# Kernel optimization log

Measured on AMD Instinct MI355X. Metric: run time of the kernel, lower is better.

## Reference

```python
import jax, jax.numpy as jnp
import numpy as np

EPS = 1e-06


def _conv1x1(x, W, b):
    # x: [B,C,H,W], W: [O,C], b: [O] -> [B,O,H,W]
    return jnp.einsum('oc,bchw->bohw', W, x) + b[None, :, None, None]


def _l2_norm(x):
    # normalize over channel dim (-2) per position, matching torch.norm(p=2, dim=-2)
    return x / jnp.linalg.norm(x, axis=-2, keepdims=True)


def setup_inputs() -> dict:
    key = jax.random.key(0)
    ks = jax.random.split(key, 8)
    B, C, H, W = 8, 512, 64, 64
    Cq = C // 8
    s = 0.02
    return {
        'x': jax.random.normal(ks[0], (B, C, H, W), jnp.float32),
        'Wq': jax.random.normal(ks[1], (Cq, C), jnp.float32) * s,
        'bq': jax.random.normal(ks[2], (Cq,), jnp.float32) * s,
        'Wk': jax.random.normal(ks[3], (Cq, C), jnp.float32) * s,
        'bk': jax.random.normal(ks[4], (Cq,), jnp.float32) * s,
        'Wv': jax.random.normal(ks[5], (C, C), jnp.float32) * s,
        'bv': jax.random.normal(ks[6], (C,), jnp.float32) * s,
        'gamma': jax.random.normal(ks[7], (1,), jnp.float32),
    }


def reference(x, Wq, bq, Wk, bk, Wv, bv, gamma):
    B, C, H, W = x.shape
    N = H * W
    Q = _conv1x1(x, Wq, bq).reshape(B, -1, N)   # [B,C',N]
    K = _conv1x1(x, Wk, bk).reshape(B, -1, N)   # [B,C',N]
    V = _conv1x1(x, Wv, bv).reshape(B, C, N)    # [B,C,N]

    Qn = _l2_norm(Q).transpose(0, 2, 1)         # [B,N,C']
    Kn = _l2_norm(K)                            # [B,C',N]

    # taylor denominator: 1 / (N + Q . (sum_n K + eps))
    tailor_sum = 1.0 / (N + jnp.einsum('bnc,bc->bn', Qn, Kn.sum(-1) + EPS))  # [B,N]

    value_sum = V.sum(-1)                        # [B,C]
    matrix = jnp.einsum('bmn,bcn->bmc', Kn, V)   # [B,C',C]
    matrix_sum = value_sum[:, :, None] + jnp.einsum('bnm,bmc->bcn', Qn, matrix)  # [B,C,N]

    weight_value = (matrix_sum * tailor_sum[:, None, :]).reshape(B, C, H, W)
    return gamma * weight_value
```

## Files before the change

kernel.cpp:

```cpp
#include <hip/hip_runtime.h>
#include <math.h>

#define B_   8
#define C_   512
#define CQ   64
#define N_   4096
#define EPSF 1e-6f
#define LS   40
#define LS2  72

typedef short  shortx8 __attribute__((ext_vector_type(8)));
typedef short  shortx4 __attribute__((ext_vector_type(4)));
typedef short  shortx2 __attribute__((ext_vector_type(2)));
typedef float  floatx4 __attribute__((ext_vector_type(4)));

__device__ __forceinline__ short f2bf(float f) {
    unsigned u = __builtin_bit_cast(unsigned, f);
    u += 0x7FFFu + ((u >> 16) & 1u);
    return (short)(u >> 16);
}
__device__ __forceinline__ float bf2f(short h) {
    unsigned u = ((unsigned)(unsigned short)h) << 16;
    return __builtin_bit_cast(float, u);
}
__device__ __forceinline__ shortx8 ldf8(const short* p) {
    return *(const shortx8*)p;
}

__global__ __launch_bounds__(256) void pcast(
    const float* __restrict__ Wq, const float* __restrict__ Wk,
    const float* __restrict__ Wv, short* __restrict__ Wqk, short* __restrict__ Wvb)
{
    int i = (blockIdx.x * 256 + threadIdx.x) * 4;
    float4 v; short* dst;
    if (i < 2 * CQ * C_) {
        const float* src = (i < CQ * C_) ? (Wq + i) : (Wk + i - CQ * C_);
        v = *(const float4*)src;
        dst = Wqk + i;
    } else {
        int j = i - 2 * CQ * C_;
        v = *(const float4*)(Wv + j);
        dst = Wvb + j;
    }
    const float* f = (const float*)&v;
    shortx4 o = { f2bf(f[0]), f2bf(f[1]), f2bf(f[2]), f2bf(f[3]) };
    *(shortx4*)dst = o;
}

__global__ __launch_bounds__(256, 2) void k1_qk(
    const float* __restrict__ x, const short* __restrict__ Wqk,
    const float* __restrict__ bq, const float* __restrict__ bk,
    short* __restrict__ Qnt, short* __restrict__ Kn, float* __restrict__ Ksum)
{
    const int b   = blockIdx.y;
    const int n0  = blockIdx.x * 64;
    const int tid = threadIdx.x;
    const int lane = tid & 63, wid = tid >> 6;
    const int waveM = wid >> 1, waveN = wid & 1;
    const int quad = lane >> 4, ln = lane & 15;

    __shared__ short A_l[2][128][LS];
    __shared__ short B_l[2][64][LS];
    __shared__ float bias_l[128];

    if (tid < 128) bias_l[tid] = (tid < 64) ? bq[tid] : bk[tid - 64];

    const int mA = tid >> 1, koA = (tid & 1) * 16;
    const short* Asrc = Wqk + (size_t)mA * C_;
    const int kp = tid >> 4, nq = tid & 15;
    const float* xb = x + (size_t)b * C_ * N_;

    shortx8 a0 = *(const shortx8*)(Asrc + koA);
    shortx8 a1 = *(const shortx8*)(Asrc + koA + 8);
    float4 r0, r1;
    {
        const float* Bs = xb + (size_t)(kp * 2) * N_ + n0 + nq * 4;
        r0 = *(const float4*)(Bs);
        r1 = *(const float4*)(Bs + N_);
    }

    auto stage = [&](int buf, shortx8 s0, shortx8 s1, float4 q0, float4 q1) {
        *(shortx8*)&A_l[buf][mA][koA]     = s0;
        *(shortx8*)&A_l[buf][mA][koA + 8] = s1;
        const float* f0 = (const float*)&q0;
        const float* f1 = (const float*)&q1;
#pragma unroll
        for (int i = 0; i < 4; i++) {
            shortx2 t = { f2bf(f0[i]), f2bf(f1[i]) };
            *(shortx2*)&B_l[buf][nq * 4 + i][kp * 2] = t;
        }
    };
    stage(0, a0, a1, r0, r1);
    __syncthreads();

    const floatx4 z4 = {0.f, 0.f, 0.f, 0.f};
    floatx4 acc[4][2];
#pragma unroll
    for (int mt = 0; mt < 4; mt++) { acc[mt][0] = z4; acc[mt][1] = z4; }

    int cur = 0;
    for (int it = 0; it < 16; ++it) {
        shortx8 na0, na1; float4 nr0, nr1;
        if (it < 15) {
            const int k0 = (it + 1) * 32;
            na0 = *(const shortx8*)(Asrc + k0 + koA);
            na1 = *(const shortx8*)(Asrc + k0 + koA + 8);
            const float* Bs = xb + (size_t)(k0 + kp * 2) * N_ + n0 + nq * 4;
            nr0 = *(const float4*)(Bs);
            nr1 = *(const float4*)(Bs + N_);
        }
        shortx8 af[4];
#pragma unroll
        for (int mt = 0; mt < 4; mt++)
            af[mt] = ldf8(&A_l[cur][waveM * 64 + mt * 16 + ln][quad * 8]);
#pragma unroll
        for (int nt = 0; nt < 2; nt++) {
            shortx8 bf8 = ldf8(&B_l[cur][waveN * 32 + nt * 16 + ln][quad * 8]);
#pragma unroll
            for (int mt = 0; mt < 4; mt++)
                acc[mt][nt] = __builtin_amdgcn_mfma_f32_16x16x32_bf16(af[mt], bf8, acc[mt][nt], 0, 0, 0);
        }
        if (it < 15) stage(cur ^ 1, na0, na1, nr0, nr1);
        __syncthreads();
        cur ^= 1;
    }

#pragma unroll
    for (int mt = 0; mt < 4; mt++)
#pragma unroll
        for (int r = 0; r < 4; r++) {
            float bias = bias_l[waveM * 64 + mt * 16 + quad * 4 + r];
#pragma unroll
            for (int nt = 0; nt < 2; nt++) acc[mt][nt][r] += bias;
        }
#pragma unroll
    for (int nt = 0; nt < 2; nt++) {
        float s = 0.f;
#pragma unroll
        for (int mt = 0; mt < 4; mt++)
#pragma unroll
            for (int r = 0; r < 4; r++) s += acc[mt][nt][r] * acc[mt][nt][r];
        s += __shfl_xor(s, 16);
        s += __shfl_xor(s, 32);
        float inv = rsqrtf(s);
#pragma unroll
        for (int mt = 0; mt < 4; mt++)
#pragma unroll
            for (int r = 0; r < 4; r++) acc[mt][nt][r] *= inv;
    }

    if (waveM == 0) {
        short* Qb = Qnt + (size_t)b * N_ * CQ;
#pragma unroll
        for (int nt = 0; nt < 2; nt++) {
            int n = n0 + waveN * 32 + nt * 16 + ln;
#pragma unroll
            for (int mt = 0; mt < 4; mt++) {
                shortx4 v;
#pragma unroll
                for (int r = 0; r < 4; r++) v[r] = f2bf(acc[mt][nt][r]);
                *(shortx4*)(Qb + (size_t)n * CQ + mt * 16 + quad * 4) = v;
            }
        }
    } else {
        short* Kb = Kn + (size_t)b * CQ * N_;
#pragma unroll
        for (int mt = 0; mt < 4; mt++)
#pragma unroll
            for (int r = 0; r < 4; r++) {
                int m = mt * 16 + quad * 4 + r;
                float s = 0.f;
#pragma unroll
                for (int nt = 0; nt < 2; nt++) {
                    int n = n0 + waveN * 32 + nt * 16 + ln;
                    float v = acc[mt][nt][r];
                    Kb[(size_t)m * N_ + n] = f2bf(v);
                    s += v;
                }
                s += __shfl_xor(s, 1); s += __shfl_xor(s, 2);
                s += __shfl_xor(s, 4); s += __shfl_xor(s, 8);
                if (ln == 0) atomicAdd(&Ksum[b * CQ + m], s);
            }
    }
}

__global__ __launch_bounds__(256, 2) void k2_kx(
    const float* __restrict__ x, const short* __restrict__ Kn,
    float* __restrict__ KX, float* __restrict__ xsum)
{
    const int jt = blockIdx.x, ks = blockIdx.y, b = blockIdx.z;
    const int j0 = jt * 64, nbase = ks * 512;
    const int tid = threadIdx.x;
    const int lane = tid & 63, wid = tid >> 6;
    const int quad = lane >> 4, ln = lane & 15;

    __shared__ short A_l[2][64][LS];
    __shared__ short B_l[2][64][LS];

    const int rA = tid >> 2, oA = (tid & 3) * 8;
    const short* Kb = Kn + (size_t)b * CQ * N_;
    const float* xb = x + (size_t)b * C_ * N_;
    const short* As = Kb + (size_t)rA * N_ + nbase + oA;
    const float* Bs = xb + (size_t)(j0 + rA) * N_ + nbase + oA;

    float xsacc = 0.f;

    shortx8 aC = *(const shortx8*)As;
    float4 b0 = *(const float4*)(Bs);
    float4 b1 = *(const float4*)(Bs + 4);

    auto stage = [&](int buf, shortx8 a, float4 q0, float4 q1) {
        *(shortx8*)&A_l[buf][rA][oA] = a;
        const float* f0 = (const float*)&q0;
        const float* f1 = (const float*)&q1;
        shortx8 t;
#pragma unroll
        for (int i = 0; i < 4; i++) {
            t[i]     = f2bf(f0[i]); xsacc += f0[i];
            t[i + 4] = f2bf(f1[i]); xsacc += f1[i];
        }
        *(shortx8*)&B_l[buf][rA][oA] = t;
    };
    stage(0, aC, b0, b1);
    __syncthreads();

    const floatx4 z4 = {0.f, 0.f, 0.f, 0.f};
    floatx4 acc[4] = {z4, z4, z4, z4};

    int cur = 0;
    for (int it = 0; it < 16; ++it) {
        shortx8 aN; float4 n0v, n1v;
        if (it < 15) {
            const int off = (it + 1) * 32;
            aN  = *(const shortx8*)(As + off);
            n0v = *(const float4*)(Bs + off);
            n1v = *(const float4*)(Bs + off + 4);
        }
        shortx8 af[4];
#pragma unroll
        for (int mt = 0; mt < 4; mt++)
            af[mt] = ldf8(&A_l[cur][mt * 16 + ln][quad * 8]);
        shortx8 bf8 = ldf8(&B_l[cur][wid * 16 + ln][quad * 8]);
#pragma unroll
        for (int mt = 0; mt < 4; mt++)
            acc[mt] = __builtin_amdgcn_mfma_f32_16x16x32_bf16(af[mt], bf8, acc[mt], 0, 0, 0);
        if (it < 15) stage(cur ^ 1, aN, n0v, n1v);
        __syncthreads();
        cur ^= 1;
    }

    xsacc += __shfl_xor(xsacc, 1);
    xsacc += __shfl_xor(xsacc, 2);
    if ((tid & 3) == 0) atomicAdd(&xsum[b * C_ + j0 + rA], xsacc);

    float* KXb = KX + (size_t)b * CQ * C_;
#pragma unroll
    for (int mt = 0; mt < 4; mt++)
#pragma unroll
        for (int r = 0; r < 4; r++) {
            int m = mt * 16 + quad * 4 + r;
            atomicAdd(&KXb[(size_t)m * C_ + j0 + wid * 16 + ln], acc[mt][r]);
        }
}

__global__ __launch_bounds__(256, 2) void k3_m(
    const float* __restrict__ KX, const short* __restrict__ Wvb,
    const float* __restrict__ bv, const float* __restrict__ Ksum,
    const float* __restrict__ xsum,
    short* __restrict__ Mt, float* __restrict__ vs)
{
    const int ct = blockIdx.x, b = blockIdx.y;
    const int c0 = ct * 64;
    const int tid = threadIdx.x;
    const int lane = tid & 63, wid = tid >> 6;
    const int quad = lane >> 4, ln = lane & 15;

    __shared__ short A_l[2][64][LS];
    __shared__ short B_l[2][64][LS];
    __shared__ float xsl[C_], Ksl[64], bvl[64], vsp[4][64];

    xsl[tid] = xsum[(size_t)b * C_ + tid];
    xsl[tid + 256] = xsum[(size_t)b * C_ + tid + 256];
    if (tid < 64) { Ksl[tid] = Ksum[b * CQ + tid]; bvl[tid] = bv[c0 + tid]; }

    const int rA = tid >> 2, oA = (tid & 3) * 8;
    const short* As = Wvb + (size_t)(c0 + rA) * C_ + oA;
    const float* Bs = KX + ((size_t)b * CQ + rA) * C_ + oA;

    shortx8 aC = *(const shortx8*)As;
    float4 b0 = *(const float4*)(Bs);
    float4 b1 = *(const float4*)(Bs + 4);

    auto stage = [&](int buf, shortx8 a, float4 q0, float4 q1) {
        *(shortx8*)&A_l[buf][rA][oA] = a;
        const float* f0 = (const float*)&q0;
        const float* f1 = (const float*)&q1;
        shortx8 t;
#pragma unroll
        for (int i = 0; i < 4; i++) { t[i] = f2bf(f0[i]); t[i + 4] = f2bf(f1[i]); }
        *(shortx8*)&B_l[buf][rA][oA] = t;
    };
    stage(0, aC, b0, b1);
    __syncthreads();

    const floatx4 z4 = {0.f, 0.f, 0.f, 0.f};
    floatx4 acc[4] = {z4, z4, z4, z4};
    float vsacc = 0.f;
    const int cv = tid & 63;

    int cur = 0;
    for (int it = 0; it < 16; ++it) {
        shortx8 aN; float4 n0v, n1v;
        if (it < 15) {
            const int off = (it + 1) * 32;
            aN  = *(const shortx8*)(As + off);
            n0v = *(const float4*)(Bs + off);
            n1v = *(const float4*)(Bs + off + 4);
        }
        shortx8 af[4];
#pragma unroll
        for (int ct2 = 0; ct2 < 4; ct2++)
            af[ct2] = ldf8(&A_l[cur][ct2 * 16 + ln][quad * 8]);
        shortx8 bf8 = ldf8(&B_l[cur][wid * 16 + ln][quad * 8]);
#pragma unroll
        for (int ct2 = 0; ct2 < 4; ct2++)
            acc[ct2] = __builtin_amdgcn_mfma_f32_16x16x32_bf16(af[ct2], bf8, acc[ct2], 0, 0, 0);
#pragma unroll
        for (int jj = 0; jj < 8; jj++)
            vsacc += bf2f(A_l[cur][cv][wid * 8 + jj]) * xsl[it * 32 + wid * 8 + jj];
        if (it < 15) stage(cur ^ 1, aN, n0v, n1v);
        __syncthreads();
        cur ^= 1;
    }

    vsp[wid][cv] = vsacc;
    __syncthreads();
    if (tid < 64)
        vs[(size_t)b * C_ + c0 + tid] =
            vsp[0][tid] + vsp[1][tid] + vsp[2][tid] + vsp[3][tid] + (float)N_ * bvl[tid];

    const int m = wid * 16 + ln;
    const float ksm = Ksl[m];
    short* Mb = Mt + (size_t)b * C_ * CQ;
#pragma unroll
    for (int ct2 = 0; ct2 < 4; ct2++)
#pragma unroll
        for (int r = 0; r < 4; r++) {
            int c = ct2 * 16 + quad * 4 + r;
            Mb[(size_t)(c0 + c) * CQ + m] = f2bf(acc[ct2][r] + ksm * bvl[c]);
        }
}

__global__ __launch_bounds__(256, 2) void k4_out(
    const short* __restrict__ Qnt, const short* __restrict__ Mt,
    const float* __restrict__ vs, const float* __restrict__ Ksum,
    const float* __restrict__ gamma, float* __restrict__ out)
{
    const int nt = blockIdx.x, ct = blockIdx.y, b = blockIdx.z;
    const int n0 = nt * 128, c0 = ct * 128;
    const int tid = threadIdx.x;
    const int lane = tid & 63, wid = tid >> 6;
    const int waveC = wid >> 1, waveN = wid & 1;
    const int quad = lane >> 4, ln = lane & 15;

    __shared__ short A_l[128][LS2];
    __shared__ short B_l[128][LS2];
    __shared__ float tsl[128], vsl[128], Ks_l[64];

    {
        int c = tid >> 1, h = tid & 1;
        const short* src = Mt + ((size_t)b * C_ + c0 + c) * CQ + h * 32;
#pragma unroll
        for (int q = 0; q < 4; q++)
            *(shortx8*)&A_l[c][h * 32 + q * 8] = *(const shortx8*)(src + q * 8);
    }
    {
        int n = tid >> 1, h = tid & 1;
        const short* src = Qnt + ((size_t)b * N_ + n0 + n) * CQ + h * 32;
#pragma unroll
        for (int q = 0; q < 4; q++)
            *(shortx8*)&B_l[n][h * 32 + q * 8] = *(const shortx8*)(src + q * 8);
    }
    if (tid < 64)  Ks_l[tid] = Ksum[b * CQ + tid];
    if (tid < 128) vsl[tid]  = vs[(size_t)b * C_ + c0 + tid];
    __syncthreads();

    if (tid < 128) {
        const short* row = B_l[tid];
        float s = 0.f;
#pragma unroll
        for (int m = 0; m < 64; m++) s += bf2f(row[m]) * (Ks_l[m] + EPSF);
        tsl[tid] = 1.f / ((float)N_ + s);
    }
    __syncthreads();

    const floatx4 z4 = {0.f, 0.f, 0.f, 0.f};
    floatx4 acc[4][4];
#pragma unroll
    for (int i = 0; i < 4; i++)
#pragma unroll
        for (int j = 0; j < 4; j++) acc[i][j] = z4;

#pragma unroll
    for (int kc = 0; kc < 2; kc++) {
        shortx8 af[4];
#pragma unroll
        for (int ct2 = 0; ct2 < 4; ct2++)
            af[ct2] = ldf8(&A_l[waveC * 64 + ct2 * 16 + ln][kc * 32 + quad * 8]);
#pragma unroll
        for (int nt2 = 0; nt2 < 4; nt2++) {
            shortx8 bf8 = ldf8(&B_l[waveN * 64 + nt2 * 16 + ln][kc * 32 + quad * 8]);
#pragma unroll
            for (int ct2 = 0; ct2 < 4; ct2++)
                acc[ct2][nt2] = __builtin_amdgcn_mfma_f32_16x16x32_bf16(af[ct2], bf8, acc[ct2][nt2], 0, 0, 0);
        }
    }

    const float g = gamma[0];
    float* ob = out + (size_t)b * C_ * N_;
#pragma unroll
    for (int ct2 = 0; ct2 < 4; ct2++)
#pragma unroll
        for (int r = 0; r < 4; r++) {
            int cl = waveC * 64 + ct2 * 16 + quad * 4 + r;
            float vc = vsl[cl];
#pragma unroll
            for (int nt2 = 0; nt2 < 4; nt2++) {
                int nl = waveN * 64 + nt2 * 16 + ln;
                ob[(size_t)(c0 + cl) * N_ + n0 + nl] = g * tsl[nl] * (vc + acc[ct2][nt2][r]);
            }
        }
}

extern "C" void kernel_launch(void* const* d_in, const int* in_sizes, int n_in,
                              void* d_out, int out_size, void* d_ws, size_t ws_size,
                              hipStream_t stream)
{
    (void)in_sizes; (void)n_in; (void)out_size; (void)ws_size;
    const float* x     = (const float*)d_in[0];
    const float* Wq    = (const float*)d_in[1];
    const float* bq    = (const float*)d_in[2];
    const float* Wk    = (const float*)d_in[3];
    const float* bk    = (const float*)d_in[4];
    const float* Wv    = (const float*)d_in[5];
    const float* bv    = (const float*)d_in[6];
    const float* gamma = (const float*)d_in[7];
    float* out = (float*)d_out;

    short* Qnt = (short*)d_ws;
    short* Kn  = Qnt + (size_t)B_ * N_ * CQ;
    float* Ksum = (float*)(Kn + (size_t)B_ * CQ * N_);
    float* xsum = Ksum + B_ * CQ;
    float* KX   = xsum + B_ * C_;
    short* Mt   = (short*)(KX + (size_t)B_ * CQ * C_);
    float* vs   = (float*)(Mt + (size_t)B_ * C_ * CQ);
    short* Wqk  = (short*)(vs + B_ * C_);
    short* Wvb  = Wqk + 2 * CQ * C_;

    size_t zbytes = (size_t)(B_ * CQ + B_ * C_ + B_ * CQ * C_) * 4;
    hipMemsetAsync(Ksum, 0, zbytes, stream);

    pcast <<<dim3(320),      256, 0, stream>>>(Wq, Wk, Wv, Wqk, Wvb);
    k1_qk <<<dim3(64, 8),    256, 0, stream>>>(x, Wqk, bq, bk, Qnt, Kn, Ksum);
    k2_kx <<<dim3(8, 8, 8),  256, 0, stream>>>(x, Kn, KX, xsum);
    k3_m  <<<dim3(8, 8),     256, 0, stream>>>(KX, Wvb, bv, Ksum, xsum, Mt, vs);
    k4_out<<<dim3(32, 4, 8), 256, 0, stream>>>(Qnt, Mt, vs, Ksum, gamma, out);
}
```

Measured before the change: 184.0 us.

## Stage full x tile in LDS upfront and read weights directly from global in k1/k2

k1_qk and k2_kx no longer run a double-buffered K loop with a sync every step. They first load and convert the whole x slab (all 512 K values) into a large padded LDS buffer, sync once, then run the MFMA loop, fetching the A operand (Wqk or Kn) straight from global or cache into registers. This removes 16 barriers per block and the A-operand LDS staging. In exchange it uses about 70KB of LDS per block, which may cut occupancy, and it gives up overlap between global loads and MFMA. k4_out's launch bound is also raised to 3 blocks per CU.

```diff
diff --git a/kernel.cpp b/kernel.cpp
--- a/kernel.cpp
+++ b/kernel.cpp
@@ -8,11 +8,13 @@
 #define EPSF 1e-6f
 #define LS   40
 #define LS2  72
+#define LSF  552
 
 typedef short  shortx8 __attribute__((ext_vector_type(8)));
 typedef short  shortx4 __attribute__((ext_vector_type(4)));
 typedef short  shortx2 __attribute__((ext_vector_type(2)));
 typedef float  floatx4 __attribute__((ext_vector_type(4)));
+typedef float  floatx2 __attribute__((ext_vector_type(2)));
 
 __device__ __forceinline__ short f2bf(float f) {
     unsigned u = __builtin_bit_cast(unsigned, f);
@@ -59,70 +61,48 @@
     const int waveM = wid >> 1, waveN = wid & 1;
     const int quad = lane >> 4, ln = lane & 15;
 
-    __shared__ short A_l[2][128][LS];
-    __shared__ short B_l[2][64][LS];
+    __shared__ __attribute__((aligned(16))) short B_l[64][LSF];
     __shared__ float bias_l[128];
 
     if (tid < 128) bias_l[tid] = (tid < 64) ? bq[tid] : bk[tid - 64];
 
-    const int mA = tid >> 1, koA = (tid & 1) * 16;
-    const short* Asrc = Wqk + (size_t)mA * C_;
-    const int kp = tid >> 4, nq = tid & 15;
+    const int nq = tid & 15, kp = tid >> 4;
     const float* xb = x + (size_t)b * C_ * N_;
-
-    shortx8 a0 = *(const shortx8*)(Asrc + koA);
-    shortx8 a1 = *(const shortx8*)(Asrc + koA + 8);
-    float4 r0, r1;
-    {
-        const float* Bs = xb + (size_t)(kp * 2) * N_ + n0 + nq * 4;
-        r0 = *(const float4*)(Bs);
-        r1 = *(const float4*)(Bs + N_);
-    }
-
-    auto stage = [&](int buf, shortx8 s0, shortx8 s1, float4 q0, float4 q1) {
-        *(shortx8*)&A_l[buf][mA][koA]     = s0;
-        *(shortx8*)&A_l[buf][mA][koA + 8] = s1;
-        const float* f0 = (const float*)&q0;
-        const float* f1 = (const float*)&q1;
-#pragma unroll
-        for (int i = 0; i < 4; i++) {
-            shortx2 t = { f2bf(f0[i]), f2bf(f1[i]) };
-            *(shortx2*)&B_l[buf][nq * 4 + i][kp * 2] = t;
-        }
-    };
-    stage(0, a0, a1, r0, r1);
-    __syncthreads();
-
+#pragma unroll 4
+    for (int i = 0; i < 16; i++) {
+        const int k = kp * 2 + 32 * i;
+        const float* p = xb + (size_t)k * N_ + n0 + nq * 4;
+        float4 r0 = *(const float4*)(p);
+        float4 r1 = *(const float4*)(p + N_);
+        const float* f0 = (const float*)&r0;
+        const float* f1 = (const float*)&r1;
+#pragma unroll
+        for (int j = 0; j < 4; j++) {
+            shortx2 t = { f2bf(f0[j]), f2bf(f1[j]) };
+            *(shortx2*)&B_l[nq * 4 + j][k] = t;
+        }
+    }
+    __syncthreads();
+
+    const short* Ab = Wqk + (size_t)(waveM * 64 + ln) * C_ + quad * 8;
     const floatx4 z4 = {0.f, 0.f, 0.f, 0.f};
     floatx4 acc[4][2];
 #pragma unroll
     for (int mt = 0; mt < 4; mt++) { acc[mt][0] = z4; acc[mt][1] = z4; }
 
-    int cur = 0;
-    for (int it = 0; it < 16; ++it) {
-        shortx8 na0, na1; float4 nr0, nr1;
-        if (it < 15) {
-            const int k0 = (it + 1) * 32;
-            na0 = *(const shortx8*)(Asrc + k0 + koA);
-            na1 = *(const shortx8*)(Asrc + k0 + koA + 8);
-            const float* Bs = xb + (size_t)(k0 + kp * 2) * N_ + n0 + nq * 4;
-            nr0 = *(const float4*)(Bs);
-            nr1 = *(const float4*)(Bs + N_);
-        }
+#pragma unroll 4
+    for (int kc = 0; kc < 16; ++kc) {
         shortx8 af[4];
 #pragma unroll
         for (int mt = 0; mt < 4; mt++)
-            af[mt] = ldf8(&A_l[cur][waveM * 64 + mt * 16 + ln][quad * 8]);
+            af[mt] = ldf8(Ab + (size_t)mt * 16 * C_ + kc * 32);
 #pragma unroll
         for (int nt = 0; nt < 2; nt++) {
-            shortx8 bf8 = ldf8(&B_l[cur][waveN * 32 + nt * 16 + ln][quad * 8]);
+            shortx8 bf8 = ldf8(&B_l[waveN * 32 + nt * 16 + ln][kc * 32 + quad * 8]);
 #pragma unroll
             for (int mt = 0; mt < 4; mt++)
                 acc[mt][nt] = __builtin_amdgcn_mfma_f32_16x16x32_bf16(af[mt], bf8, acc[mt][nt], 0, 0, 0);
         }
-        if (it < 15) stage(cur ^ 1, na0, na1, nr0, nr1);
-        __syncthreads();
-        cur ^= 1;
     }
 
 #pragma unroll
@@ -194,16 +174,84 @@
     const int lane = tid & 63, wid = tid >> 6;
     const int quad = lane >> 4, ln = lane & 15;
 
+    __shared__ __attribute__((aligned(16))) short B_l[64][LSF];
+
+    const int rA = tid >> 2, oA = (tid & 3) * 8;
+    const float* xb = x + (size_t)b * C_ * N_;
+    const float* Bs = xb + (size_t)(j0 + rA) * N_ + nbase;
+
+    float xsacc = 0.f;
+#pragma unroll 4
+    for (int i = 0; i < 16; i++) {
+        const int n = oA + 32 * i;
+        float4 b0 = *(const float4*)(Bs + n);
+        float4 b1 = *(const float4*)(Bs + n + 4);
+        const float* f0 = (const float*)&b0;
+        const float* f1 = (const float*)&b1;
+        shortx8 t;
+#pragma unroll
+        for (int q = 0; q < 4; q++) {
+            t[q]     = f2bf(f0[q]); xsacc += f0[q];
+            t[q + 4] = f2bf(f1[q]); xsacc += f1[q];
+        }
+        *(shortx8*)&B_l[rA][n] = t;
+    }
+    __syncthreads();
+
+    const short* Kb = Kn + (size_t)b * CQ * N_;
+    const short* Ab = Kb + (size_t)ln * N_ + nbase + quad * 8;
+    const floatx4 z4 = {0.f, 0.f, 0.f, 0.f};
+    floatx4 acc[4] = {z4, z4, z4, z4};
+
+#pragma unroll 4
+    for (int kc = 0; kc < 16; ++kc) {
+        shortx8 af[4];
+#pragma unroll
+        for (int mt = 0; mt < 4; mt++)
+            af[mt] = ldf8(Ab + (size_t)mt * 16 * N_ + kc * 32);
+        shortx8 bf8 = ldf8(&B_l[wid * 16 + ln][kc * 32 + quad * 8]);
+#pragma unroll
+        for (int mt = 0; mt < 4; mt++)
+            acc[mt] = __builtin_amdgcn_mfma_f32_16x16x32_bf16(af[mt], bf8, acc[mt], 0, 0, 0);
+    }
+
+    xsacc += __shfl_xor(xsacc, 1);
+    xsacc += __shfl_xor(xsacc, 2);
+    if ((tid & 3) == 0) atomicAdd(&xsum[b * C_ + j0 + rA], xsacc);
+
+    float* KXb = KX + (size_t)b * CQ * C_;
+#pragma unroll
+    for (int mt = 0; mt < 4; mt++)
+#pragma unroll
+        for (int r = 0; r < 4; r++) {
+            int m = mt * 16 + quad * 4 + r;
+            atomicAdd(&KXb[(size_t)m * C_ + j0 + wid * 16 + ln], acc[mt][r]);
+        }
+}
+
+__global__ __launch_bounds__(256, 2) void k3_m(
+    const float* __restrict__ KX, const short* __restrict__ Wvb,
+    const float* __restrict__ bv, const float* __restrict__ Ksum,
+    const float* __restrict__ xsum,
+    short* __restrict__ Mt, float* __restrict__ vs)
+{
+    const int ct = blockIdx.x, b = blockIdx.y;
+    const int c0 = ct * 64;
+    const int tid = threadIdx.x;
+    const int lane = tid & 63, wid = tid >> 6;
+    const int quad = lane >> 4, ln = lane & 15;
+
     __shared__ short A_l[2][64][LS];
     __shared__ short B_l[2][64][LS];
+    __shared__ float xsl[C_], Ksl[64], bvl[64], vsp[4][64];
+
+    xsl[tid] = xsum[(size_t)b * C_ + tid];
+    xsl[tid + 256] = xsum[(size_t)b * C_ + tid + 256];
+    if (tid < 64) { Ksl[tid] = Ksum[b * CQ + tid]; bvl[tid] = bv[c0 + tid]; }
 
     const int rA = tid >> 2, oA = (tid & 3) * 8;
-    const short* Kb = Kn + (size_t)b * CQ * N_;
-    const float* xb = x + (size_t)b * C_ * N_;
-    const short* As = Kb + (size_t)rA * N_ + nbase + oA;
-    const float* Bs = xb + (size_t)(j0 + rA) * N_ + nbase + oA;
-
-    float xsacc = 0.f;
+    const short* As = Wvb + (size_t)(c0 + rA) * C_ + oA;
+    const float* Bs = KX + ((size_t)b * CQ + rA) * C_ + oA;
 
     shortx8 aC = *(const shortx8*)As;
     float4 b0 = *(const float4*)(Bs);
@@ -215,10 +263,7 @@
         const float* f1 = (const float*)&q1;
         shortx8 t;
 #pragma unroll
-        for (int i = 0; i < 4; i++) {
-            t[i]     = f2bf(f0[i]); xsacc += f0[i];
-            t[i + 4] = f2bf(f1[i]); xsacc += f1[i];
-        }
+        for (int i = 0; i < 4; i++) { t[i] = f2bf(f0[i]); t[i + 4] = f2bf(f1[i]); }
         *(shortx8*)&B_l[buf][rA][oA] = t;
     };
     stage(0, aC, b0, b1);
@@ -226,6 +271,8 @@
 
     const floatx4 z4 = {0.f, 0.f, 0.f, 0.f};
     floatx4 acc[4] = {z4, z4, z4, z4};
+    float vsacc = 0.f;
+    const int cv = tid & 63;
 
     int cur = 0;
     for (int it = 0; it < 16; ++it) {
@@ -238,87 +285,6 @@
         }
         shortx8 af[4];
 #pragma unroll
-        for (int mt = 0; mt < 4; mt++)
-            af[mt] = ldf8(&A_l[cur][mt * 16 + ln][quad * 8]);
-        shortx8 bf8 = ldf8(&B_l[cur][wid * 16 + ln][quad * 8]);
-#pragma unroll
-        for (int mt = 0; mt < 4; mt++)
-            acc[mt] = __builtin_amdgcn_mfma_f32_16x16x32_bf16(af[mt], bf8, acc[mt], 0, 0, 0);
-        if (it < 15) stage(cur ^ 1, aN, n0v, n1v);
-        __syncthreads();
-        cur ^= 1;
-    }
-
-    xsacc += __shfl_xor(xsacc, 1);
-    xsacc += __shfl_xor(xsacc, 2);
-    if ((tid & 3) == 0) atomicAdd(&xsum[b * C_ + j0 + rA], xsacc);
-
-    float* KXb = KX + (size_t)b * CQ * C_;
-#pragma unroll
-    for (int mt = 0; mt < 4; mt++)
-#pragma unroll
-        for (int r = 0; r < 4; r++) {
-            int m = mt * 16 + quad * 4 + r;
-            atomicAdd(&KXb[(size_t)m * C_ + j0 + wid * 16 + ln], acc[mt][r]);
-        }
-}
-
-__global__ __launch_bounds__(256, 2) void k3_m(
-    const float* __restrict__ KX, const short* __restrict__ Wvb,
-    const float* __restrict__ bv, const float* __restrict__ Ksum,
-    const float* __restrict__ xsum,
-    short* __restrict__ Mt, float* __restrict__ vs)
-{
-    const int ct = blockIdx.x, b = blockIdx.y;
-    const int c0 = ct * 64;
-    const int tid = threadIdx.x;
-    const int lane = tid & 63, wid = tid >> 6;
-    const int quad = lane >> 4, ln = lane & 15;
-
-    __shared__ short A_l[2][64][LS];
-    __shared__ short B_l[2][64][LS];
-    __shared__ float xsl[C_], Ksl[64], bvl[64], vsp[4][64];
-
-    xsl[tid] = xsum[(size_t)b * C_ + tid];
-    xsl[tid + 256] = xsum[(size_t)b * C_ + tid + 256];
-    if (tid < 64) { Ksl[tid] = Ksum[b * CQ + tid]; bvl[tid] = bv[c0 + tid]; }
-
-    const int rA = tid >> 2, oA = (tid & 3) * 8;
-    const short* As = Wvb + (size_t)(c0 + rA) * C_ + oA;
-    const float* Bs = KX + ((size_t)b * CQ + rA) * C_ + oA;
-
-    shortx8 aC = *(const shortx8*)As;
-    float4 b0 = *(const float4*)(Bs);
-    float4 b1 = *(const float4*)(Bs + 4);
-
-    auto stage = [&](int buf, shortx8 a, float4 q0, float4 q1) {
-        *(shortx8*)&A_l[buf][rA][oA] = a;
-        const float* f0 = (const float*)&q0;
-        const float* f1 = (const float*)&q1;
-        shortx8 t;
-#pragma unroll
-        for (int i = 0; i < 4; i++) { t[i] = f2bf(f0[i]); t[i + 4] = f2bf(f1[i]); }
-        *(shortx8*)&B_l[buf][rA][oA] = t;
-    };
-    stage(0, aC, b0, b1);
-    __syncthreads();
-
-    const floatx4 z4 = {0.f, 0.f, 0.f, 0.f};
-    floatx4 acc[4] = {z4, z4, z4, z4};
-    float vsacc = 0.f;
-    const int cv = tid & 63;
-
-    int cur = 0;
-    for (int it = 0; it < 16; ++it) {
-        shortx8 aN; float4 n0v, n1v;
-        if (it < 15) {
-            const int off = (it + 1) * 32;
-            aN  = *(const shortx8*)(As + off);
-            n0v = *(const float4*)(Bs + off);
-            n1v = *(const float4*)(Bs + off + 4);
-        }
-        shortx8 af[4];
-#pragma unroll
         for (int ct2 = 0; ct2 < 4; ct2++)
             af[ct2] = ldf8(&A_l[cur][ct2 * 16 + ln][quad * 8]);
         shortx8 bf8 = ldf8(&B_l[cur][wid * 16 + ln][quad * 8]);
@@ -351,7 +317,7 @@
         }
 }
 
-__global__ __launch_bounds__(256, 2) void k4_out(
+__global__ __launch_bounds__(256, 3) void k4_out(
     const short* __restrict__ Qnt, const short* __restrict__ Mt,
     const float* __restrict__ vs, const float* __restrict__ Ksum,
     const float* __restrict__ gamma, float* __restrict__ out)
```

Result: slower. 198.8 us (+8.0%).

## Replace KX atomics with split-K partial buffers and split k3 reduction

Applied to the files above, without the earlier changes.

k2 now writes each K-split's partial KX tile to its own buffer instead of using float atomicAdd into a shared KX, which removes atomic contention and the memset of KX. k3 sums the eight partials while loading and is split along the reduction dimension into four slices, giving four times as many blocks. A new k3b kernel then reduces the four partial M and value-sum buffers, adds the bias terms and converts M to bf16. In exchange there is more workspace traffic, redundant partial reads in k3 and one extra kernel launch.

```diff
diff --git a/kernel.cpp b/kernel.cpp
--- a/kernel.cpp
+++ b/kernel.cpp
@@ -186,7 +186,7 @@
 
 __global__ __launch_bounds__(256, 2) void k2_kx(
     const float* __restrict__ x, const short* __restrict__ Kn,
-    float* __restrict__ KX, float* __restrict__ xsum)
+    float* __restrict__ KXp, float* __restrict__ xsum)
 {
     const int jt = blockIdx.x, ks = blockIdx.y, b = blockIdx.z;
     const int j0 = jt * 64, nbase = ks * 512;
@@ -253,43 +253,57 @@
     xsacc += __shfl_xor(xsacc, 2);
     if ((tid & 3) == 0) atomicAdd(&xsum[b * C_ + j0 + rA], xsacc);
 
-    float* KXb = KX + (size_t)b * CQ * C_;
+    float* KXb = KXp + ((size_t)b * 8 + ks) * CQ * C_;
 #pragma unroll
     for (int mt = 0; mt < 4; mt++)
 #pragma unroll
         for (int r = 0; r < 4; r++) {
             int m = mt * 16 + quad * 4 + r;
-            atomicAdd(&KXb[(size_t)m * C_ + j0 + wid * 16 + ln], acc[mt][r]);
+            KXb[(size_t)m * C_ + j0 + wid * 16 + ln] = acc[mt][r];
         }
 }
 
 __global__ __launch_bounds__(256, 2) void k3_m(
-    const float* __restrict__ KX, const short* __restrict__ Wvb,
-    const float* __restrict__ bv, const float* __restrict__ Ksum,
+    const float* __restrict__ KXp, const short* __restrict__ Wvb,
     const float* __restrict__ xsum,
-    short* __restrict__ Mt, float* __restrict__ vs)
-{
-    const int ct = blockIdx.x, b = blockIdx.y;
-    const int c0 = ct * 64;
+    float* __restrict__ Mtp, float* __restrict__ vsp2)
+{
+    const int ct = blockIdx.x, js = blockIdx.y, b = blockIdx.z;
+    const int c0 = ct * 64, jb = js * 128;
     const int tid = threadIdx.x;
     const int lane = tid & 63, wid = tid >> 6;
     const int quad = lane >> 4, ln = lane & 15;
 
     __shared__ short A_l[2][64][LS];
     __shared__ short B_l[2][64][LS];
-    __shared__ float xsl[C_], Ksl[64], bvl[64], vsp[4][64];
-
-    xsl[tid] = xsum[(size_t)b * C_ + tid];
-    xsl[tid + 256] = xsum[(size_t)b * C_ + tid + 256];
-    if (tid < 64) { Ksl[tid] = Ksum[b * CQ + tid]; bvl[tid] = bv[c0 + tid]; }
+    __shared__ float xsl[128], vsp[4][64];
+
+    if (tid < 128) xsl[tid] = xsum[(size_t)b * C_ + jb + tid];
 
     const int rA = tid >> 2, oA = (tid & 3) * 8;
-    const short* As = Wvb + (size_t)(c0 + rA) * C_ + oA;
-    const float* Bs = KX + ((size_t)b * CQ + rA) * C_ + oA;
+    const short* As = Wvb + (size_t)(c0 + rA) * C_ + jb + oA;
+    const float* Bs = KXp + ((size_t)b * 8 * CQ + rA) * C_ + jb + oA;
+    const size_t PS = (size_t)CQ * C_;
+
+    auto loadB = [&](int off, float4& o0, float4& o1) {
+        float s0[4] = {0.f, 0.f, 0.f, 0.f}, s1[4] = {0.f, 0.f, 0.f, 0.f};
+#pragma unroll
+        for (int p = 0; p < 8; p++) {
+            const float* q = Bs + p * PS + off;
+            float4 u0 = *(const float4*)(q);
+            float4 u1 = *(const float4*)(q + 4);
+            const float* g0 = (const float*)&u0;
+            const float* g1 = (const float*)&u1;
+#pragma unroll
+            for (int e = 0; e < 4; e++) { s0[e] += g0[e]; s1[e] += g1[e]; }
+        }
+        o0 = make_float4(s0[0], s0[1], s0[2], s0[3]);
+        o1 = make_float4(s1[0], s1[1], s1[2], s1[3]);
+    };
 
     shortx8 aC = *(const shortx8*)As;
-    float4 b0 = *(const float4*)(Bs);
-    float4 b1 = *(const float4*)(Bs + 4);
+    float4 b0, b1;
+    loadB(0, b0, b1);
 
     auto stage = [&](int buf, shortx8 a, float4 q0, float4 q1) {
         *(shortx8*)&A_l[buf][rA][oA] = a;
@@ -309,13 +323,12 @@
     const int cv = tid & 63;
 
     int cur = 0;
-    for (int it = 0; it < 16; ++it) {
+    for (int it = 0; it < 4; ++it) {
         shortx8 aN; float4 n0v, n1v;
-        if (it < 15) {
+        if (it < 3) {
             const int off = (it + 1) * 32;
-            aN  = *(const shortx8*)(As + off);
-            n0v = *(const float4*)(Bs + off);
-            n1v = *(const float4*)(Bs + off + 4);
+            aN = *(const shortx8*)(As + off);
+            loadB(off, n0v, n1v);
         }
         shortx8 af[4];
 #pragma unroll
@@ -328,7 +341,7 @@
 #pragma unroll
         for (int jj = 0; jj < 8; jj++)
             vsacc += bf2f(A_l[cur][cv][wid * 8 + jj]) * xsl[it * 32 + wid * 8 + jj];
-        if (it < 15) stage(cur ^ 1, aN, n0v, n1v);
+        if (it < 3) stage(cur ^ 1, aN, n0v, n1v);
         __syncthreads();
         cur ^= 1;
     }
@@ -336,19 +349,55 @@
     vsp[wid][cv] = vsacc;
     __syncthreads();
     if (tid < 64)
-        vs[(size_t)b * C_ + c0 + tid] =
-            vsp[0][tid] + vsp[1][tid] + vsp[2][tid] + vsp[3][tid] + (float)N_ * bvl[tid];
+        vsp2[((size_t)b * 4 + js) * C_ + c0 + tid] =
+            vsp[0][tid] + vsp[1][tid] + vsp[2][tid] + vsp[3][tid];
 
     const int m = wid * 16 + ln;
-    const float ksm = Ksl[m];
-    short* Mb = Mt + (size_t)b * C_ * CQ;
+    float* Mb = Mtp + ((size_t)b * 4 + js) * C_ * CQ;
 #pragma unroll
     for (int ct2 = 0; ct2 < 4; ct2++)
 #pragma unroll
         for (int r = 0; r < 4; r++) {
             int c = ct2 * 16 + quad * 4 + r;
-            Mb[(size_t)(c0 + c) * CQ + m] = f2bf(acc[ct2][r] + ksm * bvl[c]);
-        }
+            Mb[(size_t)(c0 + c) * CQ + m] = acc[ct2][r];
+        }
+}
+
+__global__ __launch_bounds__(256) void k3b(
+    const float* __restrict__ Mtp, const float* __restrict__ vsp2,
+    const float* __restrict__ Ksum, const float* __restrict__ bv,
+    short* __restrict__ Mt, float* __restrict__ vs)
+{
+    const int cb = blockIdx.x, b = blockIdx.y;
+    const int c0 = cb * 16;
+    const int tid = threadIdx.x;
+    const int c = c0 + (tid >> 4), m0 = (tid & 15) * 4;
+    const size_t PS = (size_t)C_ * CQ;
+
+    const float* base = Mtp + (size_t)b * 4 * PS + (size_t)c * CQ + m0;
+    float s[4] = {0.f, 0.f, 0.f, 0.f};
+#pragma unroll
+    for (int p = 0; p < 4; p++) {
+        float4 u = *(const float4*)(base + p * PS);
+        const float* g = (const float*)&u;
+#pragma unroll
+        for (int e = 0; e < 4; e++) s[e] += g[e];
+    }
+    const float bvc = bv[c];
+    shortx4 o;
+#pragma unroll
+    for (int r = 0; r < 4; r++)
+        o[r] = f2bf(s[r] + Ksum[b * CQ + m0 + r] * bvc);
+    *(shortx4*)(Mt + ((size_t)b * C_ + c) * CQ + m0) = o;
+
+    if (tid < 16) {
+        const int cc = c0 + tid;
+        float v = 0.f;
+#pragma unroll
+        for (int p = 0; p < 4; p++)
+            v += vsp2[((size_t)b * 4 + p) * C_ + cc];
+        vs[(size_t)b * C_ + cc] = v + (float)N_ * bv[cc];
+    }
 }
 
 __global__ __launch_bounds__(256, 2) void k4_out(
@@ -447,22 +496,25 @@
     const float* gamma = (const float*)d_in[7];
     float* out = (float*)d_out;
 
-    short* Qnt = (short*)d_ws;
-    short* Kn  = Qnt + (size_t)B_ * N_ * CQ;
+    short* Qnt  = (short*)d_ws;
+    short* Kn   = Qnt + (size_t)B_ * N_ * CQ;
     float* Ksum = (float*)(Kn + (size_t)B_ * CQ * N_);
     float* xsum = Ksum + B_ * CQ;
-    float* KX   = xsum + B_ * C_;
-    short* Mt   = (short*)(KX + (size_t)B_ * CQ * C_);
+    float* KXp  = xsum + B_ * C_;
+    float* Mtp  = KXp + (size_t)B_ * 8 * CQ * C_;
+    float* vsp2 = Mtp + (size_t)B_ * 4 * C_ * CQ;
+    short* Mt   = (short*)(vsp2 + (size_t)B_ * 4 * C_);
     float* vs   = (float*)(Mt + (size_t)B_ * C_ * CQ);
     short* Wqk  = (short*)(vs + B_ * C_);
     short* Wvb  = Wqk + 2 * CQ * C_;
 
-    size_t zbytes = (size_t)(B_ * CQ + B_ * C_ + B_ * CQ * C_) * 4;
+    size_t zbytes = (size_t)(B_ * CQ + B_ * C_) * 4;
     hipMemsetAsync(Ksum, 0, zbytes, stream);
 
     pcast <<<dim3(320),      256, 0, stream>>>(Wq, Wk, Wv, Wqk, Wvb);
     k1_qk <<<dim3(64, 8),    256, 0, stream>>>(x, Wqk, bq, bk, Qnt, Kn, Ksum);
-    k2_kx <<<dim3(8, 8, 8),  256, 0, stream>>>(x, Kn, KX, xsum);
-    k3_m  <<<dim3(8, 8),     256, 0, stream>>>(KX, Wvb, bv, Ksum, xsum, Mt, vs);
+    k2_kx <<<dim3(8, 8, 8),  256, 0, stream>>>(x, Kn, KXp, xsum);
+    k3_m  <<<dim3(8, 4, 8),  256, 0, stream>>>(KXp, Wvb, xsum, Mtp, vsp2);
+    k3b   <<<dim3(32, 8),    256, 0, stream>>>(Mtp, vsp2, Ksum, bv, Mt, vs);
     k4_out<<<dim3(32, 4, 8), 256, 0, stream>>>(Qnt, Mt, vs, Ksum, gamma, out);
 }
```

Measured after the change: 188.8 us. +2.6%, slower.
